# Optimization experiments

Measured on AMD Instinct MI355X. Metric: run time of the kernel, lower is better.

## Reference

```python
import jax, jax.numpy as jnp
import numpy as np

DIM = 4096
HEADS = 32
HD = DIM // HEADS  # 128
SEQ = 2048
BSZ = 2
ALEN = 10
ROPE_THETA = 10000.0


def _make_freqs(seq, hd):
    inv = 1.0 / (ROPE_THETA ** (np.arange(0, hd, 2, dtype=np.float32) / hd))
    t = np.arange(seq, dtype=np.float32)
    ang = np.outer(t, inv)  # [seq, hd/2]
    return jnp.asarray(np.cos(ang)), jnp.asarray(np.sin(ang))


def setup_inputs() -> dict:
    key = jax.random.key(0)
    ks = jax.random.split(key, 8)
    s = 1.0 / np.sqrt(DIM)
    x = jax.random.normal(ks[0], (BSZ, SEQ, DIM), jnp.float32)
    wq = jax.random.normal(ks[1], (DIM, DIM), jnp.float32) * s  # [in, out]
    wk = jax.random.normal(ks[2], (DIM, DIM), jnp.float32) * s
    wv = jax.random.normal(ks[3], (DIM, DIM), jnp.float32) * s
    wo = jax.random.normal(ks[4], (DIM, DIM), jnp.float32) * s
    gate = 0.1 * jax.random.normal(ks[5], (1, HEADS, 1, 1), jnp.float32)
    adapter = jax.random.normal(ks[6], (1, ALEN, DIM), jnp.float32)
    freqs_cos, freqs_sin = _make_freqs(SEQ, HD)
    # causal additive mask, start_pos = 0
    mask = jnp.triu(jnp.full((1, 1, SEQ, SEQ), -1e9, jnp.float32), k=1)
    return {"x": x, "wq": wq, "wk": wk, "wv": wv, "wo": wo, "gate": gate,
            "adapter": adapter, "freqs_cos": freqs_cos, "freqs_sin": freqs_sin,
            "mask": mask, "start_pos": 0, "random_init": 0}


def _rope(t, cos, sin):
    # t: [b, s, H, hd]; cos/sin: [s, hd/2] -> broadcast (1, s, 1, hd/2)
    b, s, h, hd = t.shape
    t2 = t.reshape(b, s, h, hd // 2, 2)
    tr, ti = t2[..., 0], t2[..., 1]
    c = cos[None, :, None, :]
    sn = sin[None, :, None, :]
    orr = tr * c - ti * sn
    oi = tr * sn + ti * c
    return jnp.stack([orr, oi], axis=-1).reshape(b, s, h, hd)


def reference(x, wq, wk, wv, wo, gate, adapter, freqs_cos, freqs_sin, mask,
              start_pos, random_init):
    bsz, seqlen, dim = x.shape
    hd = 2 * freqs_cos.shape[-1]
    H = dim // hd
    L = adapter.shape[1]
    scale = 1.0 / jnp.sqrt(jnp.float32(hd))

    xq = (x @ wq).reshape(bsz, seqlen, H, hd)
    xk = (x @ wk).reshape(bsz, seqlen, H, hd)
    xv = (x @ wv).reshape(bsz, seqlen, H, hd)

    xq = _rope(xq, freqs_cos, freqs_sin)
    xk = _rope(xk, freqs_cos, freqs_sin)

    # adapter prefix K/V (no RoPE), shared across batch
    ak = (adapter @ wk).reshape(1, L, H, hd)  # [1, L, H, hd]
    av = (adapter @ wv).reshape(1, L, H, hd)

    # scores: normal keys masked causally; adapter keys unmasked (extra zeros)
    scores_n = jnp.einsum('bqhd,bkhd->bhqk', xq, xk) * scale + mask
    scores_a = jnp.einsum('bqhd,lhd->bhql', xq, ak[0]) * scale

    if random_init:
        # joint softmax over [adapter | normal] keys
        sc = jax.nn.softmax(jnp.concatenate([scores_a, scores_n], axis=-1), axis=-1)
        pa, pn = sc[..., :L], sc[..., L:]
    else:
        pa = jnp.tanh(gate) * jax.nn.softmax(scores_a, axis=-1)
        pn = jax.nn.softmax(scores_n, axis=-1)

    out = (jnp.einsum('bhql,lhd->bqhd', pa, av[0])
           + jnp.einsum('bhqk,bkhd->bqhd', pn, xv))
    out = out.reshape(bsz, seqlen, H * hd)
    return out @ wo
```

## Files before the change

### kernel.cpp

```cpp
#include <hip/hip_runtime.h>
#include <hip/hip_bf16.h>
#include <cstdint>

typedef float  f32x4  __attribute__((ext_vector_type(4)));
typedef __bf16 bf16x8 __attribute__((ext_vector_type(8)));
typedef __bf16 bf16x4 __attribute__((ext_vector_type(4)));
typedef __bf16 bf16x2 __attribute__((ext_vector_type(2)));

#define AS1 __attribute__((address_space(1)))
#define AS3 __attribute__((address_space(3)))

static constexpr int D   = 4096;
static constexpr int SEQ = 2048;
static constexpr int MX  = 4224;

__device__ __forceinline__ void gload_lds16(const void* g, void* l) {
  __builtin_amdgcn_global_load_lds((AS1 void*)(g), (AS3 void*)(l), 16, 0, 0);
}

__device__ __forceinline__ f32x4 mfma16(bf16x8 a, bf16x8 b, f32x4 c) {
  return __builtin_amdgcn_mfma_f32_16x16x32_bf16(a, b, c, 0, 0, 0);
}

__device__ __forceinline__ int xcd_chunk(int orig, int nwg) {
  int q = nwg >> 3, r = nwg & 7;
  int xcd = orig & 7, pos = orig >> 3;
  return (xcd < r ? xcd * (q + 1) : r * (q + 1) + (xcd - r) * q) + pos;
}

#define BARF() asm volatile("s_barrier" ::: "memory")

__global__ __launch_bounds__(256) void transpose_cast(const float* __restrict__ W,
                                                      __bf16* __restrict__ WT) {
  __shared__ float tile[64][65];
  const int t  = threadIdx.x;
  const int r0 = blockIdx.x * 64;
  const int c0 = blockIdx.y * 64;
#pragma unroll
  for (int p = 0; p < 4; ++p) {
    int e = p * 1024 + t * 4;
    int row = e >> 6, col = e & 63;
    f32x4 v = *(const f32x4*)(W + (size_t)(r0 + row) * D + c0 + col);
#pragma unroll
    for (int i = 0; i < 4; ++i) tile[row][col + i] = v[i];
  }
  __syncthreads();
#pragma unroll
  for (int p = 0; p < 2; ++p) {
    int e = p * 2048 + t * 8;
    int orow = e >> 6, ocol = e & 63;
    bf16x8 o;
#pragma unroll
    for (int i = 0; i < 8; ++i) o[i] = (__bf16)tile[ocol + i][orow];
    *(bf16x8*)(WT + (size_t)(c0 + orow) * D + r0 + ocol) = o;
  }
}

__global__ __launch_bounds__(256) void build_xa(const float* __restrict__ x,
                                                const float* __restrict__ ad,
                                                __bf16* __restrict__ xa) {
  int idx = blockIdx.x * 256 + threadIdx.x;
  int e = idx * 4;
  int row = e >> 12, col = e & 4095;
  f32x4 v = {};
  if (row < 4096)      v = *(const f32x4*)(x + (size_t)row * D + col);
  else if (row < 4106) v = *(const f32x4*)(ad + (size_t)(row - 4096) * D + col);
  bf16x4 o;
#pragma unroll
  for (int i = 0; i < 4; ++i) o[i] = (__bf16)v[i];
  *(bf16x4*)(xa + (size_t)row * D + col) = o;
}

template <int MODE>
__global__ __launch_bounds__(512, 2) void gemm256(const __bf16* __restrict__ A,
                                                  const __bf16* __restrict__ BT,
                                                  void* __restrict__ O0,
                                                  void* __restrict__ O1,
                                                  void* __restrict__ O2,
                                                  int Mt) {
  __shared__ __bf16 lds[65536];
  const int tid = threadIdx.x;
  const int wv = tid >> 6, ln = tid & 63;
  const int lg = ln >> 4, lr = ln & 15;

  const int nwg = gridDim.x;
  const int wgid = xcd_chunk(blockIdx.x, nwg);
  const int m0 = (wgid % Mt) * 256;
  const int n0 = (wgid / Mt) * 256;
  const int wm = (wv >> 2) * 128, wn = (wv & 3) * 64;

  auto stageHalf = [&](int k, int mat, int half) {
    const int slot = k & 1;
    const int kt = k * 64;
    const __bf16* base = mat ? BT + (size_t)(n0 + half * 128) * 4096
                             : A  + (size_t)(m0 + half * 128) * 4096;
#pragma unroll
    for (int i = 0; i < 2; ++i) {
      int c = i * 512 + tid;
      int r = c >> 3;
      int ch = (c & 7) ^ (r & 7);
      gload_lds16(base + (size_t)r * 4096 + kt + ch * 8,
                  lds + slot * 32768 + mat * 16384 + half * 8192 +
                      (i * 512 + wv * 64) * 8);
    }
  };

  f32x4 acc[8][4] = {};
  bf16x8 aLo[4][2], aHi[4][2], bLo[2][2], bHi[2][2];

  stageHalf(0, 0, 0);
  stageHalf(0, 1, 0);
  stageHalf(0, 0, 1);
  stageHalf(0, 1, 1);

  for (int k = 0; k < 64; ++k) {
    const int slot = k & 1;
    const __bf16* pA = lds + slot * 32768;
    const __bf16* pB = lds + slot * 32768 + 16384;
    const bool pf = (k + 1 < 64);

    auto rdA = [&](int mi, int kk) -> bf16x8 {
      int r = wm + mi * 16 + lr;
      int R = r & 127;
      int cw = (kk * 4 + lg) ^ (R & 7);
      return *(const bf16x8*)(pA + (r >> 7) * 8192 + R * 64 + cw * 8);
    };
    auto rdB = [&](int ni, int kk) -> bf16x8 {
      int n = wn + ni * 16 + lr;
      int R = n & 127;
      int cw = (kk * 4 + lg) ^ (R & 7);
      return *(const bf16x8*)(pB + (n >> 7) * 8192 + R * 64 + cw * 8);
    };

    if (pf) stageHalf(k + 1, 0, 0);
    if (pf) asm volatile("s_waitcnt vmcnt(2)" ::: "memory");
    else    asm volatile("s_waitcnt vmcnt(0)" ::: "memory");
    BARF();
#pragma unroll
    for (int mi = 0; mi < 4; ++mi)
#pragma unroll
      for (int kk = 0; kk < 2; ++kk) aLo[mi][kk] = rdA(mi, kk);
#pragma unroll
    for (int ni = 0; ni < 2; ++ni)
#pragma unroll
      for (int kk = 0; kk < 2; ++kk) bLo[ni][kk] = rdB(ni, kk);
    __builtin_amdgcn_s_setprio(1);
#pragma unroll
    for (int kk = 0; kk < 2; ++kk)
#pragma unroll
      for (int mi = 0; mi < 4; ++mi)
#pragma unroll
        for (int ni = 0; ni < 2; ++ni)
          acc[mi][ni] = mfma16(aLo[mi][kk], bLo[ni][kk], acc[mi][ni]);
    __builtin_amdgcn_s_setprio(0);
    BARF();

    if (pf) stageHalf(k + 1, 1, 0);
#pragma unroll
    for (int mi = 0; mi < 4; ++mi)
#pragma unroll
      for (int kk = 0; kk < 2; ++kk) aHi[mi][kk] = rdA(mi + 4, kk);
    BARF();
    __builtin_amdgcn_s_setprio(1);
#pragma unroll
    for (int kk = 0; kk < 2; ++kk)
#pragma unroll
      for (int mi = 0; mi < 4; ++mi)
#pragma unroll
        for (int ni = 0; ni < 2; ++ni)
          acc[mi + 4][ni] = mfma16(aHi[mi][kk], bLo[ni][kk], acc[mi + 4][ni]);
    __builtin_amdgcn_s_setprio(0);
    BARF();

    if (pf) stageHalf(k + 1, 0, 1);
#pragma unroll
    for (int ni = 0; ni < 2; ++ni)
#pragma unroll
      for (int kk = 0; kk < 2; ++kk) bHi[ni][kk] = rdB(ni + 2, kk);
    BARF();
    __builtin_amdgcn_s_setprio(1);
#pragma unroll
    for (int kk = 0; kk < 2; ++kk)
#pragma unroll
      for (int mi = 0; mi < 4; ++mi)
#pragma unroll
        for (int ni = 0; ni < 2; ++ni)
          acc[mi + 4][ni + 2] = mfma16(aHi[mi][kk], bHi[ni][kk], acc[mi + 4][ni + 2]);
    __builtin_amdgcn_s_setprio(0);
    BARF();

    if (pf) stageHalf(k + 1, 1, 1);
    BARF();
    __builtin_amdgcn_s_setprio(1);
#pragma unroll
    for (int kk = 0; kk < 2; ++kk)
#pragma unroll
      for (int mi = 0; mi < 4; ++mi)
#pragma unroll
        for (int ni = 0; ni < 2; ++ni)
          acc[mi][ni + 2] = mfma16(aLo[mi][kk], bHi[ni][kk], acc[mi][ni + 2]);
    __builtin_amdgcn_s_setprio(0);
    BARF();
  }

  if constexpr (MODE == 0) {
    const int sel = n0 >> 12;
    __bf16* out = (sel == 0) ? (__bf16*)O0 : (sel == 1) ? (__bf16*)O1 : (__bf16*)O2;
    const int colb = n0 & 4095;
#pragma unroll
    for (int mi = 0; mi < 8; ++mi)
#pragma unroll
      for (int ni = 0; ni < 4; ++ni)
#pragma unroll
        for (int j = 0; j < 4; ++j) {
          int row = m0 + wm + mi * 16 + lg * 4 + j;
          int col = colb + wn + ni * 16 + lr;
          out[(size_t)row * 4096 + col] = (__bf16)acc[mi][ni][j];
        }
  } else {
    float* out = (float*)O0;
#pragma unroll
    for (int mi = 0; mi < 8; ++mi)
#pragma unroll
      for (int ni = 0; ni < 4; ++ni)
#pragma unroll
        for (int j = 0; j < 4; ++j) {
          int row = m0 + wm + mi * 16 + lg * 4 + j;
          int col = n0 + wn + ni * 16 + lr;
          out[(size_t)row * 4096 + col] = acc[mi][ni][j];
        }
  }
}

__global__ __launch_bounds__(256) void gemm_adapter(const __bf16* __restrict__ xa,
                                                    const __bf16* __restrict__ BT,
                                                    __bf16* __restrict__ kb,
                                                    __bf16* __restrict__ vb) {
  const int tid = threadIdx.x;
  const int wv = tid >> 6, ln = tid & 63;
  const int lg = ln >> 4, lr = ln & 15;
  const int col0 = blockIdx.x * 256 + wv * 64;
  f32x4 acc[4] = {};
  for (int kt = 0; kt < 4096; kt += 32) {
    bf16x8 a = *(const bf16x8*)(xa + (size_t)(4096 + lr) * 4096 + kt + lg * 8);
#pragma unroll
    for (int ni = 0; ni < 4; ++ni) {
      bf16x8 b = *(const bf16x8*)(BT + (size_t)(col0 + ni * 16 + lr) * 4096 +
                                  kt + lg * 8);
      acc[ni] = mfma16(a, b, acc[ni]);
    }
  }
#pragma unroll
  for (int ni = 0; ni < 4; ++ni)
#pragma unroll
    for (int j = 0; j < 4; ++j) {
      int row = 4096 + lg * 4 + j;
      int col = col0 + ni * 16 + lr;
      __bf16* out = (col < 4096) ? kb : vb;
      out[(size_t)row * 4096 + (col & 4095)] = (__bf16)acc[ni][j];
    }
}

__global__ __launch_bounds__(256) void rope_kernel(__bf16* __restrict__ q,
                                                   __bf16* __restrict__ k,
                                                   const float* __restrict__ fc,
                                                   const float* __restrict__ fs) {
  int row = blockIdx.x;
  __bf16* buf = blockIdx.y ? k : q;
  int t = threadIdx.x;
  int s = row & (SEQ - 1);
  int jb = (t & 7) * 8;
  const float* cp = fc + s * 64 + jb;
  const float* sp = fs + s * 64 + jb;
  __bf16* p = buf + (size_t)row * D + t * 16;
  bf16x8 v0 = *(const bf16x8*)p;
  bf16x8 v1 = *(const bf16x8*)(p + 8);
  bf16x8 o0, o1;
#pragma unroll
  for (int i = 0; i < 4; ++i) {
    float C = cp[i], Sn = sp[i];
    float re = (float)v0[2 * i], im = (float)v0[2 * i + 1];
    o0[2 * i]     = (__bf16)(re * C - im * Sn);
    o0[2 * i + 1] = (__bf16)(re * Sn + im * C);
  }
#pragma unroll
  for (int i = 0; i < 4; ++i) {
    float C = cp[4 + i], Sn = sp[4 + i];
    float re = (float)v1[2 * i], im = (float)v1[2 * i + 1];
    o1[2 * i]     = (__bf16)(re * C - im * Sn);
    o1[2 * i + 1] = (__bf16)(re * Sn + im * C);
  }
  *(bf16x8*)p = o0;
  *(bf16x8*)(p + 8) = o1;
}

__global__ __launch_bounds__(256) void transpose_v(const __bf16* __restrict__ V,
                                                   __bf16* __restrict__ VT) {
  __shared__ __bf16 tile[64][72];
  const int t  = threadIdx.x;
  const int r0 = blockIdx.x * 64;
  const int c0 = blockIdx.y * 64;
#pragma unroll
  for (int p = 0; p < 2; ++p) {
    int e = p * 2048 + t * 8;
    int row = e >> 6, col = e & 63;
    bf16x8 v8 = *(const bf16x8*)(V + (size_t)(r0 + row) * D + c0 + col);
#pragma unroll
    for (int i = 0; i < 8; ++i) tile[row][col + i] = v8[i];
  }
  __syncthreads();
#pragma unroll
  for (int p = 0; p < 2; ++p) {
    int e = p * 2048 + t * 8;
    int orow = e >> 6, ocol = e & 63;
    bf16x8 o;
#pragma unroll
    for (int i = 0; i < 8; ++i) o[i] = tile[ocol + i][orow];
    *(bf16x8*)(VT + (size_t)(c0 + orow) * MX + r0 + ocol) = o;
  }
}

__global__ __launch_bounds__(256) void attn_kernel(const __bf16* __restrict__ Q,
                                                   const __bf16* __restrict__ K,
                                                   const __bf16* __restrict__ VT,
                                                   const float* __restrict__ gate,
                                                   __bf16* __restrict__ Out) {
  __shared__ __bf16 Ks[2][64 * 128];
  __shared__ __bf16 Vs[2][128 * 64];
  __shared__ __bf16 Ps[4][32 * 64];

  const int tid = threadIdx.x;
  const int wv = tid >> 6, ln = tid & 63;
  const int lg = ln >> 4, lr = ln & 15;

  const int wgid = xcd_chunk(blockIdx.x, 512);
  const int px = wgid & 7;
  const int hb = wgid >> 3;
  const int h = hb & 31, b = hb >> 5;

  const float scale = 0.08838834764831845f;
  const float g = tanhf(gate[h]);

  auto stage = [&](int t, int buf) {
    const int kv0 = t * 64;
#pragma unroll
    for (int j = 0; j < 4; ++j) {
      int c = wv * 256 + j * 64 + ln;
      int rk = c >> 4, sck = (c & 15) ^ (rk & 7);
      gload_lds16(K + (size_t)(b * SEQ + kv0 + rk) * D + h * 128 + sck * 8,
                  Ks[buf] + (wv * 256 + j * 64) * 8);
      int rv = c >> 3, scv = (c & 7) ^ (rv & 7);
      gload_lds16(VT + (size_t)(h * 128 + rv) * MX + b * SEQ + kv0 + scv * 8,
                  Vs[buf] + (wv * 256 + j * 64) * 8);
    }
  };

  auto run_supertile = [&](int qt) {
    const int q0 = qt * 128;
    const int qbase = b * SEQ + q0 + wv * 32;

    bf16x8 qf[2][4];
#pragma unroll
    for (int mi = 0; mi < 2; ++mi)
#pragma unroll
      for (int kd = 0; kd < 4; ++kd)
        qf[mi][kd] = *(const bf16x8*)(Q + (size_t)(qbase + mi * 16 + lr) * D +
                                      h * 128 + kd * 32 + lg * 8);

    f32x4 O[2][8] = {};
    float mI2[2], lI2[2];
#pragma unroll
    for (int mi = 0; mi < 2; ++mi) { mI2[mi] = -1e30f; lI2[mi] = 0.f; }

    const int ntiles = 2 * qt + 2;
    stage(0, 0);

    for (int t = 0; t < ntiles; ++t) {
      const int cur = t & 1;
      const int kv0 = t * 64;
      if (t + 1 < ntiles) {
        stage(t + 1, cur ^ 1);
        asm volatile("s_waitcnt vmcnt(8)" ::: "memory");
      } else {
        asm volatile("s_waitcnt vmcnt(0)" ::: "memory");
      }
      __builtin_amdgcn_s_barrier();
      __builtin_amdgcn_sched_barrier(0);

      f32x4 S[2][4] = {};
      __builtin_amdgcn_s_setprio(1);
#pragma unroll
      for (int kd = 0; kd < 4; ++kd) {
        bf16x8 kf[4];
#pragma unroll
        for (int nf = 0; nf < 4; ++nf) {
          int kr = nf * 16 + lr;
          kf[nf] = *(const bf16x8*)(Ks[cur] + kr * 128 +
                                    (((kd * 4 + lg) ^ (kr & 7)) * 8));
        }
#pragma unroll
        for (int mi = 0; mi < 2; ++mi)
#pragma unroll
          for (int nf = 0; nf < 4; ++nf)
            S[mi][nf] = mfma16(kf[nf], qf[mi][kd], S[mi][nf]);
      }
      __builtin_amdgcn_s_setprio(0);

      float r2[2]; int grew = 0;
#pragma unroll
      for (int mi = 0; mi < 2; ++mi) {
        const int qg = q0 + wv * 32 + mi * 16 + lr;
        float mo = mI2[mi];
        float mt = -3e38f;
#pragma unroll
        for (int nf = 0; nf < 4; ++nf)
#pragma unroll
          for (int j = 0; j < 4; ++j) {
            int kvg = kv0 + nf * 16 + lg * 4 + j;
            float s = S[mi][nf][j] * scale;
            s = (kvg > qg) ? -1e30f : s;
            S[mi][nf][j] = s;
            mt = fmaxf(mt, s);
          }
        mt = fmaxf(mt, __shfl_xor(mt, 16));
        mt = fmaxf(mt, __shfl_xor(mt, 32));
        float mn = fmaxf(mo, mt);
        float ps = 0.f;
#pragma unroll
        for (int nf = 0; nf < 4; ++nf)
#pragma unroll
          for (int j = 0; j < 4; ++j) {
            float p = __expf(S[mi][nf][j] - mn);
            S[mi][nf][j] = p;
            ps += p;
          }
        ps += __shfl_xor(ps, 16);
        ps += __shfl_xor(ps, 32);
        float r = __expf(mo - mn);
        lI2[mi] = lI2[mi] * r + ps;
        mI2[mi] = mn;
        r2[mi] = r;
        grew |= (mn > mo) ? 1 : 0;
      }
      if (__any(grew)) {
#pragma unroll
        for (int mi = 0; mi < 2; ++mi)
#pragma unroll
          for (int j = 0; j < 4; ++j) {
            float rj = __shfl(r2[mi], lg * 4 + j);
#pragma unroll
            for (int n = 0; n < 8; ++n) O[mi][n][j] *= rj;
          }
      }

#pragma unroll
      for (int mi = 0; mi < 2; ++mi) {
        int q = mi * 16 + lr;
#pragma unroll
        for (int nf = 0; nf < 4; ++nf) {
          int kv = nf * 16 + lg * 4;
          bf16x4 pk;
#pragma unroll
          for (int j = 0; j < 4; ++j) pk[j] = (__bf16)S[mi][nf][j];
          *(bf16x4*)(Ps[wv] + q * 64 + (((kv >> 3) ^ (q & 7)) * 8) + (kv & 7)) = pk;
        }
      }

      __builtin_amdgcn_s_setprio(1);
#pragma unroll
      for (int kkv = 0; kkv < 2; ++kkv) {
        bf16x8 pf[2];
#pragma unroll
        for (int mi = 0; mi < 2; ++mi) {
          int prw = mi * 16 + lr;
          pf[mi] = *(const bf16x8*)(Ps[wv] + prw * 64 +
                                    (((kkv * 4 + lg) ^ (prw & 7)) * 8));
        }
#pragma unroll
        for (int n = 0; n < 8; ++n) {
          int vr = n * 16 + lr;
          bf16x8 vf = *(const bf16x8*)(Vs[cur] + vr * 64 +
                                       (((kkv * 4 + lg) ^ (vr & 7)) * 8));
#pragma unroll
          for (int mi = 0; mi < 2; ++mi) O[mi][n] = mfma16(pf[mi], vf, O[mi][n]);
        }
      }
      __builtin_amdgcn_s_setprio(0);

      __builtin_amdgcn_s_barrier();
      __builtin_amdgcn_sched_barrier(0);
    }

#pragma unroll
    for (int mi = 0; mi < 2; ++mi) {
      float inv = 1.0f / lI2[mi];
#pragma unroll
      for (int j = 0; j < 4; ++j) {
        float invj = __shfl(inv, lg * 4 + j);
#pragma unroll
        for (int n = 0; n < 8; ++n) O[mi][n][j] *= invj;
      }
    }

    {
      f32x4 Sa[2] = {};
#pragma unroll
      for (int kd = 0; kd < 4; ++kd) {
        bf16x8 kfa = *(const bf16x8*)(K + (size_t)(2 * SEQ + lr) * D +
                                      h * 128 + kd * 32 + lg * 8);
#pragma unroll
        for (int mi = 0; mi < 2; ++mi) Sa[mi] = mfma16(kfa, qf[mi][kd], Sa[mi]);
      }
#pragma unroll
      for (int mi = 0; mi < 2; ++mi) {
        float mt = -3e38f;
#pragma unroll
        for (int j = 0; j < 4; ++j) {
          int kv = lg * 4 + j;
          float s = Sa[mi][j] * scale;
          s = (kv >= 10) ? -1e30f : s;
          Sa[mi][j] = s;
          mt = fmaxf(mt, s);
        }
        mt = fmaxf(mt, __shfl_xor(mt, 16));
        mt = fmaxf(mt, __shfl_xor(mt, 32));
        float ps = 0.f;
#pragma unroll
        for (int j = 0; j < 4; ++j) {
          float p = __expf(Sa[mi][j] - mt);
          Sa[mi][j] = p;
          ps += p;
        }
        ps += __shfl_xor(ps, 16);
        ps += __shfl_xor(ps, 32);
        float gs = g / ps;
        int q = mi * 16 + lr;
        int kv = lg * 4;
        bf16x4 pk, z = {};
#pragma unroll
        for (int j = 0; j < 4; ++j) pk[j] = (__bf16)(Sa[mi][j] * gs);
        *(bf16x4*)(Ps[wv] + q * 64 + (((kv >> 3) ^ (q & 7)) * 8) + (kv & 7)) = pk;
        int kv2 = 16 + kv;
        *(bf16x4*)(Ps[wv] + q * 64 + (((kv2 >> 3) ^ (q & 7)) * 8) + (kv2 & 7)) = z;
      }
      bf16x8 pfa[2];
#pragma unroll
      for (int mi = 0; mi < 2; ++mi) {
        int prw = mi * 16 + lr;
        pfa[mi] = *(const bf16x8*)(Ps[wv] + prw * 64 + ((lg ^ (prw & 7)) * 8));
      }
#pragma unroll
      for (int n = 0; n < 8; ++n) {
        bf16x8 vfa = *(const bf16x8*)(VT + (size_t)(h * 128 + n * 16 + lr) * MX +
                                      2 * SEQ + lg * 8);
#pragma unroll
        for (int mi = 0; mi < 2; ++mi) O[mi][n] = mfma16(pfa[mi], vfa, O[mi][n]);
      }
    }

#pragma unroll
    for (int mi = 0; mi < 2; ++mi)
#pragma unroll
      for (int n = 0; n < 8; ++n)
#pragma unroll
        for (int j = 0; j < 4; ++j)
          Out[(size_t)(qbase + mi * 16 + lg * 4 + j) * D + h * 128 + n * 16 + lr] =
              (__bf16)O[mi][n][j];
  };

  run_supertile(15 - px);
  run_supertile(px);
}

extern "C" void kernel_launch(void* const* d_in, const int* in_sizes, int n_in,
                              void* d_out, int out_size, void* d_ws, size_t ws_size,
                              hipStream_t stream) {
  const float* x    = (const float*)d_in[0];
  const float* wq   = (const float*)d_in[1];
  const float* wk   = (const float*)d_in[2];
  const float* wv   = (const float*)d_in[3];
  const float* wo   = (const float*)d_in[4];
  const float* gate = (const float*)d_in[5];
  const float* ad   = (const float*)d_in[6];
  const float* fc   = (const float*)d_in[7];
  const float* fs   = (const float*)d_in[8];

  const size_t WSZ = (size_t)D * D * 2;
  const size_t XSZ = (size_t)MX * D * 2;
  if (ws_size < 4 * WSZ + XSZ + WSZ + 3 * XSZ) return;

  char* w = (char*)d_ws;
  size_t off = 0;
  auto alloc = [&](size_t sz) { void* p = w + off; off += sz; return p; };
  __bf16* wqT = (__bf16*)alloc(WSZ);
  __bf16* wkT = (__bf16*)alloc(WSZ);
  __bf16* wvT = (__bf16*)alloc(WSZ);
  __bf16* woT = (__bf16*)alloc(WSZ);
  __bf16* xa  = (__bf16*)alloc(XSZ);
  __bf16* qb  = (__bf16*)alloc(WSZ);
  __bf16* kb  = (__bf16*)alloc(XSZ);
  __bf16* vb  = (__bf16*)alloc(XSZ);
  __bf16* vT  = (__bf16*)alloc(XSZ);
  __bf16* attn = vb;

  dim3 blk(256);
  transpose_cast<<<dim3(64, 64), blk, 0, stream>>>(wq, wqT);
  transpose_cast<<<dim3(64, 64), blk, 0, stream>>>(wk, wkT);
  transpose_cast<<<dim3(64, 64), blk, 0, stream>>>(wv, wvT);
  transpose_cast<<<dim3(64, 64), blk, 0, stream>>>(wo, woT);
  build_xa<<<dim3(16896), blk, 0, stream>>>(x, ad, xa);

  gemm256<0><<<dim3(16 * 48), dim3(512), 0, stream>>>(xa, wqT, qb, kb, vb, 16);
  gemm_adapter<<<dim3(32), blk, 0, stream>>>(xa, wkT, kb, vb);

  rope_kernel<<<dim3(4096, 2), blk, 0, stream>>>(qb, kb, fc, fs);
  transpose_v<<<dim3(66, 64), blk, 0, stream>>>(vb, vT);

  attn_kernel<<<dim3(512), blk, 0, stream>>>(qb, kb, vT, gate, attn);

  gemm256<1><<<dim3(16 * 16), dim3(512), 0, stream>>>(attn, woT, d_out, nullptr, nullptr, 16);
}
```

Before: 897.6 us.

## Deepen GEMM prefetch pipeline with reordered half-tile staging and peeled tail

```diff
diff --git a/kernel.cpp b/kernel.cpp
--- a/kernel.cpp
+++ b/kernel.cpp
@@ -108,42 +108,42 @@
   f32x4 acc[8][4] = {};
   bf16x8 aLo[4][2], aHi[4][2], bLo[2][2], bHi[2][2];
 
+  auto rdA = [&](const __bf16* pA, int mi, int kk) -> bf16x8 {
+    int r = wm + mi * 16 + lr;
+    int R = r & 127;
+    int cw = (kk * 4 + lg) ^ (R & 7);
+    return *(const bf16x8*)(pA + (r >> 7) * 8192 + R * 64 + cw * 8);
+  };
+  auto rdB = [&](const __bf16* pB, int ni, int kk) -> bf16x8 {
+    int n = wn + ni * 16 + lr;
+    int R = n & 127;
+    int cw = (kk * 4 + lg) ^ (R & 7);
+    return *(const bf16x8*)(pB + (n >> 7) * 8192 + R * 64 + cw * 8);
+  };
+
   stageHalf(0, 0, 0);
   stageHalf(0, 1, 0);
   stageHalf(0, 0, 1);
   stageHalf(0, 1, 1);
-
-  for (int k = 0; k < 64; ++k) {
+  stageHalf(1, 0, 0);
+  stageHalf(1, 1, 0);
+
+  for (int k = 0; k < 63; ++k) {
     const int slot = k & 1;
     const __bf16* pA = lds + slot * 32768;
     const __bf16* pB = lds + slot * 32768 + 16384;
-    const bool pf = (k + 1 < 64);
-
-    auto rdA = [&](int mi, int kk) -> bf16x8 {
-      int r = wm + mi * 16 + lr;
-      int R = r & 127;
-      int cw = (kk * 4 + lg) ^ (R & 7);
-      return *(const bf16x8*)(pA + (r >> 7) * 8192 + R * 64 + cw * 8);
-    };
-    auto rdB = [&](int ni, int kk) -> bf16x8 {
-      int n = wn + ni * 16 + lr;
-      int R = n & 127;
-      int cw = (kk * 4 + lg) ^ (R & 7);
-      return *(const bf16x8*)(pB + (n >> 7) * 8192 + R * 64 + cw * 8);
-    };
-
-    if (pf) stageHalf(k + 1, 0, 0);
-    if (pf) asm volatile("s_waitcnt vmcnt(2)" ::: "memory");
-    else    asm volatile("s_waitcnt vmcnt(0)" ::: "memory");
+
+    stageHalf(k + 1, 0, 1);
+    asm volatile("s_waitcnt vmcnt(8)" ::: "memory");
     BARF();
 #pragma unroll
     for (int mi = 0; mi < 4; ++mi)
 #pragma unroll
-      for (int kk = 0; kk < 2; ++kk) aLo[mi][kk] = rdA(mi, kk);
+      for (int kk = 0; kk < 2; ++kk) aLo[mi][kk] = rdA(pA, mi, kk);
 #pragma unroll
     for (int ni = 0; ni < 2; ++ni)
 #pragma unroll
-      for (int kk = 0; kk < 2; ++kk) bLo[ni][kk] = rdB(ni, kk);
+      for (int kk = 0; kk < 2; ++kk) bLo[ni][kk] = rdB(pB, ni, kk);
     __builtin_amdgcn_s_setprio(1);
 #pragma unroll
     for (int kk = 0; kk < 2; ++kk)
@@ -155,11 +155,12 @@
     __builtin_amdgcn_s_setprio(0);
     BARF();
 
-    if (pf) stageHalf(k + 1, 1, 0);
+    stageHalf(k + 1, 1, 1);
 #pragma unroll
     for (int mi = 0; mi < 4; ++mi)
 #pragma unroll
-      for (int kk = 0; kk < 2; ++kk) aHi[mi][kk] = rdA(mi + 4, kk);
+      for (int kk = 0; kk < 2; ++kk) aHi[mi][kk] = rdA(pA, mi + 4, kk);
+    asm volatile("s_waitcnt vmcnt(8)" ::: "memory");
     BARF();
     __builtin_amdgcn_s_setprio(1);
 #pragma unroll
@@ -172,11 +173,11 @@
     __builtin_amdgcn_s_setprio(0);
     BARF();
 
-    if (pf) stageHalf(k + 1, 0, 1);
+    if (k + 2 < 64) stageHalf(k + 2, 0, 0);
 #pragma unroll
     for (int ni = 0; ni < 2; ++ni)
 #pragma unroll
-      for (int kk = 0; kk < 2; ++kk) bHi[ni][kk] = rdB(ni + 2, kk);
+      for (int kk = 0; kk < 2; ++kk) bHi[ni][kk] = rdB(pB, ni + 2, kk);
     BARF();
     __builtin_amdgcn_s_setprio(1);
 #pragma unroll
@@ -189,7 +190,7 @@
     __builtin_amdgcn_s_setprio(0);
     BARF();
 
-    if (pf) stageHalf(k + 1, 1, 1);
+    if (k + 2 < 64) stageHalf(k + 2, 1, 0);
     BARF();
     __builtin_amdgcn_s_setprio(1);
 #pragma unroll
@@ -201,6 +202,46 @@
           acc[mi][ni + 2] = mfma16(aLo[mi][kk], bHi[ni][kk], acc[mi][ni + 2]);
     __builtin_amdgcn_s_setprio(0);
     BARF();
+  }
+
+  {
+    const __bf16* pA = lds + (63 & 1) * 32768;
+    const __bf16* pB = lds + (63 & 1) * 32768 + 16384;
+    asm volatile("s_waitcnt vmcnt(0)" ::: "memory");
+    BARF();
+#pragma unroll
+    for (int mi = 0; mi < 4; ++mi)
+#pragma unroll
+      for (int kk = 0; kk < 2; ++kk) aLo[mi][kk] = rdA(pA, mi, kk);
+#pragma unroll
+    for (int ni = 0; ni < 2; ++ni)
+#pragma unroll
+      for (int kk = 0; kk < 2; ++kk) bLo[ni][kk] = rdB(pB, ni, kk);
+#pragma unroll
+    for (int kk = 0; kk < 2; ++kk)
+#pragma unroll
+      for (int mi = 0; mi < 4; ++mi)
+#pragma unroll
+        for (int ni = 0; ni < 2; ++ni)
+          acc[mi][ni] = mfma16(aLo[mi][kk], bLo[ni][kk], acc[mi][ni]);
+#pragma unroll
+    for (int mi = 0; mi < 4; ++mi)
+#pragma unroll
+      for (int kk = 0; kk < 2; ++kk) aHi[mi][kk] = rdA(pA, mi + 4, kk);
+#pragma unroll
+    for (int ni = 0; ni < 2; ++ni)
+#pragma unroll
+      for (int kk = 0; kk < 2; ++kk) bHi[ni][kk] = rdB(pB, ni + 2, kk);
+#pragma unroll
+    for (int kk = 0; kk < 2; ++kk)
+#pragma unroll
+      for (int mi = 0; mi < 4; ++mi)
+#pragma unroll
+        for (int ni = 0; ni < 2; ++ni) {
+          acc[mi + 4][ni]     = mfma16(aHi[mi][kk], bLo[ni][kk], acc[mi + 4][ni]);
+          acc[mi + 4][ni + 2] = mfma16(aHi[mi][kk], bHi[ni][kk], acc[mi + 4][ni + 2]);
+          acc[mi][ni + 2]     = mfma16(aLo[mi][kk], bHi[ni][kk], acc[mi][ni + 2]);
+        }
   }
 
   if constexpr (MODE == 0) {
```

Result: faster. 850.8 us (-5.2%).
